# Kernel tuning notes

Measured on AMD Instinct MI355X. Metric: run time of the kernel, lower is better.

Reference implementation:

```python
import jax, jax.numpy as jnp
import numpy as np

N, E, G, D, H, C = 50000, 800000, 64, 128, 4, 32
EPS = 1e-5  # GraphNorm eps


def _gcn(x, W, b, src, dst, n):
    # PyG GCNConv: add self-loops (done by caller), symmetric norm D^-1/2 A D^-1/2
    xw = x @ W
    deg = jax.ops.segment_sum(jnp.ones_like(dst, dtype=xw.dtype), dst, num_segments=n)
    dinv = jnp.where(deg > 0, jax.lax.rsqrt(jnp.maximum(deg, 1e-12)), 0.0)
    norm = dinv[src] * dinv[dst]                      # [E2]
    out = jax.ops.segment_sum(xw[src] * norm[:, None], dst, num_segments=n)
    return out + b


def _gat(x, W, a_src, a_dst, b, src, dst, n):
    # PyG GATConv, heads=H, out C per head, concat, leaky_relu slope 0.2, self-loops added by caller
    h = (x @ W).reshape(n, H, C)
    es = jnp.einsum('nhc,hc->nh', h, a_src)
    ed = jnp.einsum('nhc,hc->nh', h, a_dst)
    e = jax.nn.leaky_relu(es[src] + ed[dst], 0.2)     # [E2,H]
    m = jax.ops.segment_max(e, dst, num_segments=n)   # per-dst softmax (stable)
    e = jnp.exp(e - m[dst])
    s = jax.ops.segment_sum(e, dst, num_segments=n)
    alpha = e / (s[dst] + 1e-16)
    out = jax.ops.segment_sum(h[src] * alpha[:, :, None], dst, num_segments=n)
    return out.reshape(n, H * C) + b


def _graphnorm(x, batch, w, b, ms, g):
    cnt = jnp.maximum(jax.ops.segment_sum(jnp.ones((x.shape[0],), x.dtype), batch, num_segments=g), 1.0)
    mean = jax.ops.segment_sum(x, batch, num_segments=g) / cnt[:, None]
    sub = x - ms * mean[batch]
    var = jax.ops.segment_sum(sub * sub, batch, num_segments=g) / cnt[:, None]
    return w * sub * jax.lax.rsqrt(var[batch] + EPS) + b


def setup_inputs() -> dict:
    key = jax.random.key(0)
    ks = jax.random.split(key, 40)

    def lin(k, din, dout):
        return jax.random.normal(k, (din, dout), jnp.float32) * np.float32((2.0 / (din + dout)) ** 0.5)

    inp = {
        'x': jax.random.normal(ks[0], (N, D), jnp.float32),
        'edge_index': jax.random.randint(ks[1], (2, E), 0, N, dtype=jnp.int32),
        'batch': jnp.sort(jax.random.randint(ks[2], (N,), 0, G, dtype=jnp.int32)),
        'Wp': lin(ks[3], D, D), 'bp': jnp.zeros((D,), jnp.float32),
        'Wg': lin(ks[4], D, D), 'bg': jnp.zeros((D,), jnp.float32),
        'Wa1': lin(ks[5], D, H * C), 'as1': jax.random.normal(ks[6], (H, C), jnp.float32) * 0.1,
        'ad1': jax.random.normal(ks[7], (H, C), jnp.float32) * 0.1, 'ba1': jnp.zeros((D,), jnp.float32),
        'Wa2': lin(ks[8], D, H * C), 'as2': jax.random.normal(ks[9], (H, C), jnp.float32) * 0.1,
        'ad2': jax.random.normal(ks[10], (H, C), jnp.float32) * 0.1, 'ba2': jnp.zeros((D,), jnp.float32),
        'gnw0': jnp.ones((D,), jnp.float32), 'gnb0': jnp.zeros((D,), jnp.float32), 'gns0': jnp.ones((D,), jnp.float32),
        'gnw1': jnp.ones((D,), jnp.float32), 'gnb1': jnp.zeros((D,), jnp.float32), 'gns1': jnp.ones((D,), jnp.float32),
        'gnw2': jnp.ones((D,), jnp.float32), 'gnb2': jnp.zeros((D,), jnp.float32), 'gns2': jnp.ones((D,), jnp.float32),
        'hw1': lin(ks[11], 2 * D, D), 'hb1': jnp.zeros((D,), jnp.float32),
        'hw2': lin(ks[12], D, D // 2), 'hb2': jnp.zeros((D // 2,), jnp.float32),
        'hw3': lin(ks[13], D // 2, 2), 'hb3': jnp.zeros((2,), jnp.float32),
        'nw1': lin(ks[14], D, D // 2), 'nb1': jnp.zeros((D // 2,), jnp.float32),
        'nw2': lin(ks[15], D // 2, 1), 'nb2': jnp.zeros((1,), jnp.float32),
    }
    return inp


def reference(x, edge_index, batch, Wp, bp, Wg, bg, Wa1, as1, ad1, ba1, Wa2, as2, ad2, ba2,
              gnw0, gnb0, gns0, gnw1, gnb1, gns1, gnw2, gnb2, gns2,
              hw1, hb1, hw2, hb2, hw3, hb3, nw1, nb1, nw2, nb2):
    n = x.shape[0]
    loop = jnp.arange(n, dtype=edge_index.dtype)
    src = jnp.concatenate([edge_index[0], loop])
    dst = jnp.concatenate([edge_index[1], loop])

    x = x @ Wp + bp
    h = _graphnorm(_gcn(x, Wg, bg, src, dst, n), batch, gnw0, gnb0, gns0, G)
    x = jax.nn.relu(h) + x  # dropout is identity in eval mode
    h = _graphnorm(_gat(x, Wa1, as1, ad1, ba1, src, dst, n), batch, gnw1, gnb1, gns1, G)
    x = jax.nn.relu(h) + x
    h = _graphnorm(_gat(x, Wa2, as2, ad2, ba2, src, dst, n), batch, gnw2, gnb2, gns2, G)
    x = jax.nn.relu(h) + x

    node_hub_scores = jax.nn.sigmoid((jax.nn.relu(x @ nw1 + nb1) @ nw2 + nb2)[:, 0])

    cnt = jnp.maximum(jax.ops.segment_sum(jnp.ones((n,), x.dtype), batch, num_segments=G), 1.0)
    gmean = jax.ops.segment_sum(x, batch, num_segments=G) / cnt[:, None]
    gmax = jax.ops.segment_max(x, batch, num_segments=G)
    graph_features = jnp.concatenate([gmean, gmax], axis=1)  # [G, 2D]

    z = jax.nn.relu(graph_features @ hw1 + hb1)
    z = jax.nn.relu(z @ hw2 + hb2)
    logits = z @ hw3 + hb3
    return (logits, node_hub_scores, graph_features, x)
```

## Files before the change

### kernel.cpp

```cpp
#include <hip/hip_runtime.h>
#include <cstdint>

#define D 128
#define GG 64
#define SLICES 16

typedef short bf16x8 __attribute__((ext_vector_type(8)));
typedef float f32x4 __attribute__((ext_vector_type(4)));

__device__ inline unsigned packbf2(float a, float b) {
  unsigned ua = __float_as_uint(a), ub = __float_as_uint(b);
  ua = (ua + 0x7FFFu + ((ua >> 16) & 1u)) >> 16;
  ub = (ub + 0x7FFFu + ((ub >> 16) & 1u)) >> 16;
  return ua | (ub << 16);
}
__device__ inline unsigned short bf16u(float f) {
  unsigned u = __float_as_uint(f);
  u = (u + 0x7FFFu + ((u >> 16) & 1u)) >> 16;
  return (unsigned short)u;
}
__device__ inline float2 unpackbf2(unsigned u) {
  return make_float2(__uint_as_float(u << 16), __uint_as_float(u & 0xFFFF0000u));
}

__global__ void count_edges_k(const int* __restrict__ dst, int* __restrict__ cnt, int E) {
  int e = blockIdx.x * blockDim.x + threadIdx.x;
  if (e < E) atomicAdd(&cnt[dst[e]], 1);
}

__global__ void bounds_init_k(int* __restrict__ gstart, int* __restrict__ gend) {
  int g = threadIdx.x;
  gstart[g] = 0;
  gend[g] = 0;
}

__global__ void graph_bounds_k(const int* __restrict__ batch, int* __restrict__ gstart,
                               int* __restrict__ gend, int n) {
  int i = blockIdx.x * blockDim.x + threadIdx.x;
  if (i >= n) return;
  int b = batch[i];
  if (i == 0) {
    gstart[b] = 0;
  } else {
    int pb = batch[i - 1];
    if (pb != b) { gstart[b] = i; gend[pb] = i; }
  }
  if (i == n - 1) gend[b] = n;
}

__global__ void gcnt_k(const int* __restrict__ gstart, const int* __restrict__ gend,
                       int* __restrict__ gcnt) {
  int g = threadIdx.x;
  gcnt[g] = gend[g] - gstart[g];
}

__global__ __launch_bounds__(256) void scan1_k(const int* __restrict__ cnt, int* __restrict__ rp,
                                               int* __restrict__ bsum, int n) {
  __shared__ int sd[256];
  int t = threadIdx.x;
  int i = blockIdx.x * 256 + t;
  int v = (i < n) ? cnt[i] : 0;
  sd[t] = v;
  __syncthreads();
#pragma unroll
  for (int off = 1; off < 256; off <<= 1) {
    int u = (t >= off) ? sd[t - off] : 0;
    __syncthreads();
    sd[t] += u;
    __syncthreads();
  }
  if (i < n) rp[i] = sd[t] - v;
  if (t == 255) bsum[blockIdx.x] = sd[255];
}

__global__ __launch_bounds__(256) void scan2_k(int* __restrict__ bsum, int nb) {
  __shared__ int sd[256];
  int t = threadIdx.x;
  int v = (t < nb) ? bsum[t] : 0;
  sd[t] = v;
  __syncthreads();
#pragma unroll
  for (int off = 1; off < 256; off <<= 1) {
    int u = (t >= off) ? sd[t - off] : 0;
    __syncthreads();
    sd[t] += u;
    __syncthreads();
  }
  if (t < nb) bsum[t] = sd[t] - v;
}

__global__ __launch_bounds__(256) void scan3_k(int* __restrict__ rp, const int* __restrict__ bsum,
                                               int* __restrict__ cur, int n, int E) {
  int i = blockIdx.x * 256 + threadIdx.x;
  if (i < n) {
    int r = rp[i] + bsum[blockIdx.x];
    rp[i] = r;
    cur[i] = r;
  }
  if (i == 0) rp[n] = E;
}

__global__ void fill_csr_k(const int* __restrict__ src, const int* __restrict__ dst,
                           int* __restrict__ cur, int* __restrict__ col, int E) {
  int e = blockIdx.x * blockDim.x + threadIdx.x;
  if (e >= E) return;
  int p = atomicAdd(&cur[dst[e]], 1);
  col[p] = src[e];
}

__global__ void dinv_k(const int* __restrict__ cnt, float* __restrict__ dinv, int n) {
  int i = blockIdx.x * blockDim.x + threadIdx.x;
  if (i < n) dinv[i] = rsqrtf((float)cnt[i] + 1.0f);
}

__global__ void cast_bf16_k(const float* __restrict__ in, unsigned short* __restrict__ outp, int n4) {
  int i = blockIdx.x * blockDim.x + threadIdx.x;
  if (i >= n4) return;
  float4 v = ((const float4*)in)[i];
  ushort4 o;
  o.x = bf16u(v.x); o.y = bf16u(v.y); o.z = bf16u(v.z); o.w = bf16u(v.w);
  ((ushort4*)outp)[i] = o;
}

__global__ void packB_k(const float* __restrict__ B, unsigned short* __restrict__ Bp, int ldb, int ct) {
  int idx = blockIdx.x * 256 + threadIdx.x;
  if (idx >= ct * 256) return;
  int lane = idx & 63;
  int kc = (idx >> 6) & 3;
  int c = idx >> 8;
  int kb = kc * 32 + (lane >> 4) * 8;
  int colq = c * 16 + (lane & 15);
  unsigned short o[8];
#pragma unroll
  for (int j = 0; j < 8; ++j) o[j] = bf16u(B[(size_t)(kb + j) * ldb + colq]);
  uint4 p;
  p.x = (unsigned)o[0] | ((unsigned)o[1] << 16);
  p.y = (unsigned)o[2] | ((unsigned)o[3] << 16);
  p.z = (unsigned)o[4] | ((unsigned)o[5] << 16);
  p.w = (unsigned)o[6] | ((unsigned)o[7] << 16);
  *(uint4*)&Bp[(size_t)idx * 8] = p;
}

__global__ __launch_bounds__(256) void gemm_mfma_k(const unsigned short* __restrict__ Ab,
                                                   const unsigned short* __restrict__ Bp,
                                                   const float* __restrict__ bias,
                                                   float* __restrict__ Cf,
                                                   unsigned short* __restrict__ Cb, int M) {
  __shared__ unsigned short Bs[16384];
  int t = threadIdx.x;
  for (int i = t; i < 2048; i += 256) ((uint4*)Bs)[i] = ((const uint4*)Bp)[i];
  __syncthreads();
  int w = t >> 6, lane = t & 63;
  int row0 = blockIdx.x * 64 + w * 16;
  int arow = row0 + (lane & 15);
  f32x4 acc[8];
#pragma unroll
  for (int c = 0; c < 8; ++c) acc[c] = {0.f, 0.f, 0.f, 0.f};
#pragma unroll
  for (int kc = 0; kc < 4; ++kc) {
    bf16x8 a = {0, 0, 0, 0, 0, 0, 0, 0};
    if (arow < M) a = *(const bf16x8*)&Ab[(size_t)arow * 128 + kc * 32 + (lane >> 4) * 8];
#pragma unroll
    for (int c = 0; c < 8; ++c) {
      bf16x8 b = *(const bf16x8*)&Bs[((c * 4 + kc) * 64 + lane) * 8];
      acc[c] = __builtin_amdgcn_mfma_f32_16x16x32_bf16(a, b, acc[c], 0, 0, 0);
    }
  }
  int rbase = row0 + (lane >> 4) * 4;
#pragma unroll
  for (int c = 0; c < 8; ++c) {
    int colq = c * 16 + (lane & 15);
    float bb = bias ? bias[colq] : 0.f;
#pragma unroll
    for (int r = 0; r < 4; ++r) {
      int row = rbase + r;
      if (row < M) {
        float v = acc[c][r] + bb;
        if (Cf) Cf[(size_t)row * 128 + colq] = v;
        if (Cb) Cb[(size_t)row * 128 + colq] = bf16u(v);
      }
    }
  }
}

__global__ __launch_bounds__(256) void gcn_gather_k(const unsigned* __restrict__ xwb,
                                                    const int* __restrict__ rp, const int* __restrict__ col,
                                                    const float* __restrict__ dinv, const float* __restrict__ bias,
                                                    float* __restrict__ out, int n) {
  int i = blockIdx.x * 4 + (threadIdx.x >> 6);
  if (i >= n) return;
  int lane = threadIdx.x & 63;
  int e0 = __builtin_amdgcn_readfirstlane(rp[i]);
  int e1 = __builtin_amdgcn_readfirstlane(rp[i + 1]);
  float di = dinv[i];
  float2 sv = unpackbf2(xwb[(size_t)i * 64 + lane]);
  float ax0 = sv.x * di * di, ay0 = sv.y * di * di;
  float ax1 = 0.f, ay1 = 0.f, ax2 = 0.f, ay2 = 0.f, ax3 = 0.f, ay3 = 0.f;
  int e = e0;
  for (; e + 3 < e1; e += 4) {
    int s0 = __builtin_amdgcn_readfirstlane(col[e]);
    int s1 = __builtin_amdgcn_readfirstlane(col[e + 1]);
    int s2 = __builtin_amdgcn_readfirstlane(col[e + 2]);
    int s3 = __builtin_amdgcn_readfirstlane(col[e + 3]);
    float w0 = dinv[s0] * di, w1 = dinv[s1] * di, w2 = dinv[s2] * di, w3 = dinv[s3] * di;
    float2 v0 = unpackbf2(xwb[(size_t)s0 * 64 + lane]);
    float2 v1 = unpackbf2(xwb[(size_t)s1 * 64 + lane]);
    float2 v2 = unpackbf2(xwb[(size_t)s2 * 64 + lane]);
    float2 v3 = unpackbf2(xwb[(size_t)s3 * 64 + lane]);
    ax0 += v0.x * w0; ay0 += v0.y * w0;
    ax1 += v1.x * w1; ay1 += v1.y * w1;
    ax2 += v2.x * w2; ay2 += v2.y * w2;
    ax3 += v3.x * w3; ay3 += v3.y * w3;
  }
  for (; e < e1; ++e) {
    int s0 = __builtin_amdgcn_readfirstlane(col[e]);
    float w0 = dinv[s0] * di;
    float2 v0 = unpackbf2(xwb[(size_t)s0 * 64 + lane]);
    ax0 += v0.x * w0; ay0 += v0.y * w0;
  }
  float2 bb = ((const float2*)bias)[lane];
  ((float2*)out)[(size_t)i * 64 + lane] =
      make_float2(ax0 + ax1 + ax2 + ax3 + bb.x, ay0 + ay1 + ay2 + ay3 + bb.y);
}

__global__ void attn_coef_k(const unsigned short* __restrict__ hb, const float* __restrict__ a_s,
                            const float* __restrict__ a_d, float* __restrict__ es,
                            float* __restrict__ ed, int n) {
  int idx = blockIdx.x * blockDim.x + threadIdx.x;
  if (idx >= n * 4) return;
  int node = idx >> 2, hh = idx & 3;
  const uint4* hr = (const uint4*)(hb + (size_t)node * 128 + hh * 32);
  const float4* av = (const float4*)(a_s + hh * 32);
  const float4* dv = (const float4*)(a_d + hh * 32);
  float s = 0.f, d2 = 0.f;
#pragma unroll
  for (int q = 0; q < 4; ++q) {
    uint4 u = hr[q];
    float2 p0 = unpackbf2(u.x), p1 = unpackbf2(u.y), p2 = unpackbf2(u.z), p3 = unpackbf2(u.w);
    float4 a0 = av[q * 2], a1 = av[q * 2 + 1];
    float4 d0 = dv[q * 2], d1 = dv[q * 2 + 1];
    s  += p0.x * a0.x + p0.y * a0.y + p1.x * a0.z + p1.y * a0.w
        + p2.x * a1.x + p2.y * a1.y + p3.x * a1.z + p3.y * a1.w;
    d2 += p0.x * d0.x + p0.y * d0.y + p1.x * d0.z + p1.y * d0.w
        + p2.x * d1.x + p2.y * d1.y + p3.x * d1.z + p3.y * d1.w;
  }
  es[idx] = s;
  ed[idx] = d2;
}

__global__ __launch_bounds__(256) void alpha_k(const float* __restrict__ es, const float* __restrict__ ed,
                                               const int* __restrict__ rp, const int* __restrict__ col,
                                               float* __restrict__ alpha, float* __restrict__ aself, int n) {
  int i = blockIdx.x * 4 + (threadIdx.x >> 6);
  if (i >= n) return;
  int lane = threadIdx.x & 63;
  int hh = lane >> 4, slot = lane & 15;
  int e0 = __builtin_amdgcn_readfirstlane(rp[i]);
  int e1 = __builtin_amdgcn_readfirstlane(rp[i + 1]);
  float edi = ed[i * 4 + hh];
  float esf = es[i * 4 + hh] + edi;
  esf = esf >= 0.f ? esf : 0.2f * esf;
  float m = esf;
  for (int e = e0 + slot; e < e1; e += 16) {
    int sj = col[e];
    float ev = es[sj * 4 + hh] + edi;
    ev = ev >= 0.f ? ev : 0.2f * ev;
    alpha[(size_t)e * 4 + hh] = ev;
    m = fmaxf(m, ev);
  }
#pragma unroll
  for (int off = 1; off < 16; off <<= 1) m = fmaxf(m, __shfl_xor(m, off, 64));
  float s = (slot == 0) ? __expf(esf - m) : 0.f;
  for (int e = e0 + slot; e < e1; e += 16) {
    float w = __expf(alpha[(size_t)e * 4 + hh] - m);
    alpha[(size_t)e * 4 + hh] = w;
    s += w;
  }
#pragma unroll
  for (int off = 1; off < 16; off <<= 1) s += __shfl_xor(s, off, 64);
  float winv = 1.0f / (s + 1e-16f);
  for (int e = e0 + slot; e < e1; e += 16) {
    alpha[(size_t)e * 4 + hh] *= winv;
  }
  if (slot == 0) aself[i * 4 + hh] = __expf(esf - m) * winv;
}

__global__ __launch_bounds__(256) void gat_gather_k(const unsigned* __restrict__ hfb,
                                                    const int* __restrict__ rp, const int* __restrict__ col,
                                                    const float* __restrict__ alpha, const float* __restrict__ aself,
                                                    const float* __restrict__ bias, float* __restrict__ out, int n) {
  int i = blockIdx.x * 4 + (threadIdx.x >> 6);
  if (i >= n) return;
  int lane = threadIdx.x & 63;
  int hh = lane >> 4;
  int e0 = __builtin_amdgcn_readfirstlane(rp[i]);
  int e1 = __builtin_amdgcn_readfirstlane(rp[i + 1]);
  float2 sv = unpackbf2(hfb[(size_t)i * 64 + lane]);
  float a0 = aself[i * 4 + hh];
  float ax0 = sv.x * a0, ay0 = sv.y * a0;
  float ax1 = 0.f, ay1 = 0.f, ax2 = 0.f, ay2 = 0.f, ax3 = 0.f, ay3 = 0.f;
  int e = e0;
  for (; e + 3 < e1; e += 4) {
    int s0 = __builtin_amdgcn_readfirstlane(col[e]);
    int s1 = __builtin_amdgcn_readfirstlane(col[e + 1]);
    int s2 = __builtin_amdgcn_readfirstlane(col[e + 2]);
    int s3 = __builtin_amdgcn_readfirstlane(col[e + 3]);
    float aa0 = alpha[(size_t)e * 4 + hh];
    float aa1 = alpha[(size_t)(e + 1) * 4 + hh];
    float aa2 = alpha[(size_t)(e + 2) * 4 + hh];
    float aa3 = alpha[(size_t)(e + 3) * 4 + hh];
    float2 v0 = unpackbf2(hfb[(size_t)s0 * 64 + lane]);
    float2 v1 = unpackbf2(hfb[(size_t)s1 * 64 + lane]);
    float2 v2 = unpackbf2(hfb[(size_t)s2 * 64 + lane]);
    float2 v3 = unpackbf2(hfb[(size_t)s3 * 64 + lane]);
    ax0 += v0.x * aa0; ay0 += v0.y * aa0;
    ax1 += v1.x * aa1; ay1 += v1.y * aa1;
    ax2 += v2.x * aa2; ay2 += v2.y * aa2;
    ax3 += v3.x * aa3; ay3 += v3.y * aa3;
  }
  for (; e < e1; ++e) {
    int s0 = __builtin_amdgcn_readfirstlane(col[e]);
    float aa0 = alpha[(size_t)e * 4 + hh];
    float2 v0 = unpackbf2(hfb[(size_t)s0 * 64 + lane]);
    ax0 += v0.x * aa0; ay0 += v0.y * aa0;
  }
  float2 bb = ((const float2*)bias)[lane];
  ((float2*)out)[(size_t)i * 64 + lane] =
      make_float2(ax0 + ax1 + ax2 + ax3 + bb.x, ay0 + ay1 + ay2 + ay3 + bb.y);
}

__global__ __launch_bounds__(256) void gn_stats_k(const float* __restrict__ h, const int* __restrict__ gstart,
                                                  const int* __restrict__ gcnt, float* __restrict__ gsum,
                                                  float* __restrict__ gsq) {
  int g = blockIdx.x / SLICES, sl = blockIdx.x % SLICES;
  int st = gstart[g], cn = gcnt[g];
  int d = threadIdx.x & 127, half = threadIdx.x >> 7;
  float s = 0.f, ss = 0.f;
  for (int r = sl * 2 + half; r < cn; r += 2 * SLICES) {
    float v = h[(size_t)(st + r) * D + d];
    s += v; ss += v * v;
  }
  __shared__ float l1[128], l2[128];
  if (half) { l1[d] = s; l2[d] = ss; }
  __syncthreads();
  if (!half) {
    atomicAdd(&gsum[g * D + d], s + l1[d]);
    atomicAdd(&gsq[g * D + d], ss + l2[d]);
  }
}

__global__ void gn_finalize_k(const float* __restrict__ gsum, const float* __restrict__ gsq,
                              const int* __restrict__ gcnt, const float* __restrict__ ms,
                              float* __restrict__ mean, float* __restrict__ rstd) {
  int g = blockIdx.x, d = threadIdx.x;
  float cnt = fmaxf((float)gcnt[g], 1.0f);
  float mu = gsum[g * D + d] / cnt;
  float m2 = gsq[g * D + d] / cnt;
  float s = ms[d];
  float var = m2 - (2.0f * s - s * s) * mu * mu;
  mean[g * D + d] = mu;
  rstd[g * D + d] = rsqrtf(fmaxf(var, 0.0f) + 1e-5f);
}

__global__ void gn_apply_k(const float* __restrict__ h, float* __restrict__ x,
                           unsigned short* __restrict__ xb,
                           const int* __restrict__ batch, const float* __restrict__ mean,
                           const float* __restrict__ rstd, const float* __restrict__ w,
                           const float* __restrict__ b, const float* __restrict__ ms, int n) {
  int idx = blockIdx.x * blockDim.x + threadIdx.x;
  if (idx >= n * 32) return;
  int node = idx >> 5, q = idx & 31;
  int g = batch[node];
  int d0 = q * 4;
  float4 hv = ((const float4*)h)[idx];
  float4 xv = ((const float4*)x)[idx];
  float ha[4] = {hv.x, hv.y, hv.z, hv.w};
  float xa[4] = {xv.x, xv.y, xv.z, xv.w};
  float ra[4];
#pragma unroll
  for (int j = 0; j < 4; ++j) {
    int d = d0 + j;
    float sub = ha[j] - ms[d] * mean[g * D + d];
    float v = w[d] * sub * rstd[g * D + d] + b[d];
    ra[j] = fmaxf(v, 0.f) + xa[j];
  }
  ((float4*)x)[idx] = make_float4(ra[0], ra[1], ra[2], ra[3]);
  ushort4 o;
  o.x = bf16u(ra[0]); o.y = bf16u(ra[1]); o.z = bf16u(ra[2]); o.w = bf16u(ra[3]);
  ((ushort4*)xb)[idx] = o;
}

__global__ __launch_bounds__(256) void hub_mfma_k(const unsigned short* __restrict__ Xb,
                                                  const unsigned short* __restrict__ W1p,
                                                  const float* __restrict__ nb1, const float* __restrict__ nw2,
                                                  const float* __restrict__ nb2, float* __restrict__ out, int n) {
  __shared__ unsigned short Bs[8192];
  int t = threadIdx.x;
  for (int i = t; i < 1024; i += 256) ((uint4*)Bs)[i] = ((const uint4*)W1p)[i];
  __syncthreads();
  int w = t >> 6, lane = t & 63;
  int row0 = blockIdx.x * 64 + w * 16;
  int arow = row0 + (lane & 15);
  f32x4 acc[4];
#pragma unroll
  for (int c = 0; c < 4; ++c) acc[c] = {0.f, 0.f, 0.f, 0.f};
#pragma unroll
  for (int kc = 0; kc < 4; ++kc) {
    bf16x8 a = {0, 0, 0, 0, 0, 0, 0, 0};
    if (arow < n) a = *(const bf16x8*)&Xb[(size_t)arow * 128 + kc * 32 + (lane >> 4) * 8];
#pragma unroll
    for (int c = 0; c < 4; ++c) {
      bf16x8 b = *(const bf16x8*)&Bs[((c * 4 + kc) * 64 + lane) * 8];
      acc[c] = __builtin_amdgcn_mfma_f32_16x16x32_bf16(a, b, acc[c], 0, 0, 0);
    }
  }
  float b2 = nb2[0];
  float s[4] = {0.f, 0.f, 0.f, 0.f};
#pragma unroll
  for (int c = 0; c < 4; ++c) {
    int colq = c * 16 + (lane & 15);
    float b1 = nb1[colq];
    float w2 = nw2[colq];
#pragma unroll
    for (int r = 0; r < 4; ++r) s[r] += fmaxf(acc[c][r] + b1, 0.f) * w2;
  }
#pragma unroll
  for (int off = 1; off < 16; off <<= 1) {
#pragma unroll
    for (int r = 0; r < 4; ++r) s[r] += __shfl_xor(s[r], off, 64);
  }
  if ((lane & 15) == 0) {
    int rbase = row0 + (lane >> 4) * 4;
#pragma unroll
    for (int r = 0; r < 4; ++r) {
      int row = rbase + r;
      if (row < n) out[row] = 1.0f / (1.0f + __expf(-(s[r] + b2)));
    }
  }
}

__global__ void init_maxu_k(unsigned* __restrict__ p, int n) {
  int i = blockIdx.x * blockDim.x + threadIdx.x;
  if (i < n) p[i] = 0x007FFFFFu;
}

__global__ __launch_bounds__(256) void pool_stats_k(const float* __restrict__ x, const int* __restrict__ gstart,
                                                    const int* __restrict__ gcnt, float* __restrict__ gsum,
                                                    unsigned* __restrict__ gmaxu) {
  int g = blockIdx.x / SLICES, sl = blockIdx.x % SLICES;
  int st = gstart[g], cn = gcnt[g];
  int d = threadIdx.x & 127, half = threadIdx.x >> 7;
  float s = 0.f, mx = __uint_as_float(0xFF800000u);
  for (int r = sl * 2 + half; r < cn; r += 2 * SLICES) {
    float v = x[(size_t)(st + r) * D + d];
    s += v; mx = fmaxf(mx, v);
  }
  __shared__ float l1[128], l2[128];
  if (half) { l1[d] = s; l2[d] = mx; }
  __syncthreads();
  if (!half) {
    s += l1[d];
    mx = fmaxf(mx, l2[d]);
    atomicAdd(&gsum[g * D + d], s);
    unsigned u = __float_as_uint(mx);
    u = (u & 0x80000000u) ? ~u : (u | 0x80000000u);
    atomicMax(&gmaxu[g * D + d], u);
  }
}

__global__ void pool_fin_k(const float* __restrict__ gsum, const unsigned* __restrict__ gmaxu,
                           const int* __restrict__ gcnt, float* __restrict__ gf) {
  int g = blockIdx.x, d = threadIdx.x;
  float cnt = fmaxf((float)gcnt[g], 1.0f);
  gf[g * 256 + d] = gsum[g * D + d] / cnt;
  unsigned u = gmaxu[g * D + d];
  unsigned bits = (u & 0x80000000u) ? (u ^ 0x80000000u) : ~u;
  gf[g * 256 + 128 + d] = __uint_as_float(bits);
}

__global__ __launch_bounds__(128) void mlp_k(const float* __restrict__ gf, const float* __restrict__ hw1,
                                             const float* __restrict__ hb1, const float* __restrict__ hw2,
                                             const float* __restrict__ hb2, const float* __restrict__ hw3,
                                             const float* __restrict__ hb3, float* __restrict__ logits) {
  __shared__ float sg[256], z1[128], z2[64];
  int g = blockIdx.x, t = threadIdx.x;
  sg[t] = gf[g * 256 + t];
  sg[t + 128] = gf[g * 256 + 128 + t];
  __syncthreads();
  float a = hb1[t];
  for (int k = 0; k < 256; ++k) a += sg[k] * hw1[k * 128 + t];
  z1[t] = fmaxf(a, 0.f);
  __syncthreads();
  if (t < 64) {
    float a2 = hb2[t];
    for (int k = 0; k < 128; ++k) a2 += z1[k] * hw2[k * 64 + t];
    z2[t] = fmaxf(a2, 0.f);
  }
  __syncthreads();
  if (t < 2) {
    float a3 = hb3[t];
    for (int k = 0; k < 64; ++k) a3 += z2[k] * hw3[k * 2 + t];
    logits[g * 2 + t] = a3;
  }
}

extern "C" void kernel_launch(void* const* d_in, const int* in_sizes, int n_in,
                              void* d_out, int out_size, void* d_ws, size_t ws_size,
                              hipStream_t stream) {
  const float* x_in  = (const float*)d_in[0];
  const int*   eidx  = (const int*)d_in[1];
  const int*   batch = (const int*)d_in[2];
  const float* Wp  = (const float*)d_in[3];
  const float* bp  = (const float*)d_in[4];
  const float* Wg  = (const float*)d_in[5];
  const float* bg  = (const float*)d_in[6];
  const float* Wa1 = (const float*)d_in[7];
  const float* as1 = (const float*)d_in[8];
  const float* ad1 = (const float*)d_in[9];
  const float* ba1 = (const float*)d_in[10];
  const float* Wa2 = (const float*)d_in[11];
  const float* as2 = (const float*)d_in[12];
  const float* ad2 = (const float*)d_in[13];
  const float* ba2 = (const float*)d_in[14];
  const float* gnw[3] = {(const float*)d_in[15], (const float*)d_in[18], (const float*)d_in[21]};
  const float* gnb[3] = {(const float*)d_in[16], (const float*)d_in[19], (const float*)d_in[22]};
  const float* gns[3] = {(const float*)d_in[17], (const float*)d_in[20], (const float*)d_in[23]};
  const float* hw1 = (const float*)d_in[24];
  const float* hb1 = (const float*)d_in[25];
  const float* hw2 = (const float*)d_in[26];
  const float* hb2 = (const float*)d_in[27];
  const float* hw3 = (const float*)d_in[28];
  const float* hb3 = (const float*)d_in[29];
  const float* nw1 = (const float*)d_in[30];
  const float* nb1 = (const float*)d_in[31];
  const float* nw2 = (const float*)d_in[32];
  const float* nb2 = (const float*)d_in[33];

  const int N = in_sizes[0] / D;
  const int E = in_sizes[1] / 2;
  const int* src = eidx;
  const int* dst = eidx + E;

  float* out    = (float*)d_out;
  float* logits = out;
  float* hub    = out + GG * 2;
  float* gf     = out + GG * 2 + N;
  float* X      = out + GG * 2 + N + GG * 256;

  char* wp = (char*)d_ws;
  auto alloc = [&](size_t bytes) { char* p = wp; wp += (bytes + 255) & ~(size_t)255; return p; };
  float*    B1    = (float*)alloc((size_t)N * D * 4);
  float*    B2    = (float*)alloc((size_t)N * D * 4);
  unsigned* B1h   = (unsigned*)alloc((size_t)N * (D / 2) * 4);
  unsigned short* Xb = (unsigned short*)alloc((size_t)N * D * 2);
  int*   col     = (int*)alloc((size_t)E * 4);
  int*   cnt     = (int*)alloc((size_t)N * 4);
  int*   rowp    = (int*)alloc((size_t)(N + 1) * 4);
  int*   cur     = (int*)alloc((size_t)N * 4);
  float* dinv    = (float*)alloc((size_t)N * 4);
  float* es      = (float*)alloc((size_t)N * 4 * 4);
  float* ed      = (float*)alloc((size_t)N * 4 * 4);
  float* aself   = (float*)alloc((size_t)N * 4 * 4);
  float* gsum    = (float*)alloc((size_t)GG * D * 4);
  float* gsq     = (float*)alloc((size_t)GG * D * 4);
  unsigned* gmaxu = (unsigned*)alloc((size_t)GG * D * 4);
  float* mean    = (float*)alloc((size_t)GG * D * 4);
  float* rstd    = (float*)alloc((size_t)GG * D * 4);
  int*   gcnt    = (int*)alloc((size_t)GG * 4);
  int*   gstart  = (int*)alloc((size_t)GG * 4);
  int*   gend    = (int*)alloc((size_t)GG * 4);
  int*   bsum    = (int*)alloc((size_t)256 * 4);
  unsigned short* Wpp  = (unsigned short*)alloc(16384 * 2);
  unsigned short* Wgp  = (unsigned short*)alloc(16384 * 2);
  unsigned short* Wa1p = (unsigned short*)alloc(16384 * 2);
  unsigned short* Wa2p = (unsigned short*)alloc(16384 * 2);
  unsigned short* W1p  = (unsigned short*)alloc(8192 * 2);
  float* alpha = B1;
  unsigned short* xinb = (unsigned short*)B2;
  if ((size_t)(wp - (char*)d_ws) > ws_size) return;

  const int nb = (N + 255) / 256;

  hipMemsetAsync(cnt, 0, (size_t)N * 4, stream);
  count_edges_k<<<(E + 255) / 256, 256, 0, stream>>>(dst, cnt, E);
  bounds_init_k<<<1, GG, 0, stream>>>(gstart, gend);
  graph_bounds_k<<<nb, 256, 0, stream>>>(batch, gstart, gend, N);
  gcnt_k<<<1, GG, 0, stream>>>(gstart, gend, gcnt);
  scan1_k<<<nb, 256, 0, stream>>>(cnt, rowp, bsum, N);
  scan2_k<<<1, 256, 0, stream>>>(bsum, nb);
  scan3_k<<<nb, 256, 0, stream>>>(rowp, bsum, cur, N, E);
  dinv_k<<<nb, 256, 0, stream>>>(cnt, dinv, N);
  fill_csr_k<<<(E + 255) / 256, 256, 0, stream>>>(src, dst, cur, col, E);

  packB_k<<<8, 256, 0, stream>>>(Wp, Wpp, 128, 8);
  packB_k<<<8, 256, 0, stream>>>(Wg, Wgp, 128, 8);
  packB_k<<<8, 256, 0, stream>>>(Wa1, Wa1p, 128, 8);
  packB_k<<<8, 256, 0, stream>>>(Wa2, Wa2p, 128, 8);
  packB_k<<<4, 256, 0, stream>>>(nw1, W1p, 64, 4);
  cast_bf16_k<<<(N * 32 + 255) / 256, 256, 0, stream>>>(x_in, xinb, N * 32);

  const int gemmGrid = (N + 63) / 64;
  const int aggGrid  = (N + 3) / 4;

  auto graphnorm = [&](int layer) {
    hipMemsetAsync(gsum, 0, 2 * (size_t)GG * D * 4, stream);
    gn_stats_k<<<GG * SLICES, 256, 0, stream>>>(B2, gstart, gcnt, gsum, gsq);
    gn_finalize_k<<<GG, D, 0, stream>>>(gsum, gsq, gcnt, gns[layer], mean, rstd);
    gn_apply_k<<<(N * 32 + 255) / 256, 256, 0, stream>>>(B2, X, Xb, batch, mean, rstd,
                                                         gnw[layer], gnb[layer], gns[layer], N);
  };

  gemm_mfma_k<<<gemmGrid, 256, 0, stream>>>(xinb, Wpp, bp, X, Xb, N);

  gemm_mfma_k<<<gemmGrid, 256, 0, stream>>>(Xb, Wgp, nullptr, nullptr, (unsigned short*)B1h, N);
  gcn_gather_k<<<aggGrid, 256, 0, stream>>>(B1h, rowp, col, dinv, bg, B2, N);
  graphnorm(0);

  gemm_mfma_k<<<gemmGrid, 256, 0, stream>>>(Xb, Wa1p, nullptr, nullptr, (unsigned short*)B1h, N);
  attn_coef_k<<<(N * 4 + 255) / 256, 256, 0, stream>>>((const unsigned short*)B1h, as1, ad1, es, ed, N);
  alpha_k<<<aggGrid, 256, 0, stream>>>(es, ed, rowp, col, alpha, aself, N);
  gat_gather_k<<<aggGrid, 256, 0, stream>>>(B1h, rowp, col, alpha, aself, ba1, B2, N);
  graphnorm(1);

  gemm_mfma_k<<<gemmGrid, 256, 0, stream>>>(Xb, Wa2p, nullptr, nullptr, (unsigned short*)B1h, N);
  attn_coef_k<<<(N * 4 + 255) / 256, 256, 0, stream>>>((const unsigned short*)B1h, as2, ad2, es, ed, N);
  alpha_k<<<aggGrid, 256, 0, stream>>>(es, ed, rowp, col, alpha, aself, N);
  gat_gather_k<<<aggGrid, 256, 0, stream>>>(B1h, rowp, col, alpha, aself, ba2, B2, N);
  graphnorm(2);

  hub_mfma_k<<<gemmGrid, 256, 0, stream>>>(Xb, W1p, nb1, nw2, nb2, hub, N);

  hipMemsetAsync(gsum, 0, (size_t)GG * D * 4, stream);
  init_maxu_k<<<(GG * D + 255) / 256, 256, 0, stream>>>(gmaxu, GG * D);
  pool_stats_k<<<GG * SLICES, 256, 0, stream>>>(X, gstart, gcnt, gsum, gmaxu);
  pool_fin_k<<<GG, D, 0, stream>>>(gsum, gmaxu, gcnt, gf);
  mlp_k<<<GG, 128, 0, stream>>>(gf, hw1, hb1, hw2, hb2, hw3, hb3, logits);
}
```

Baseline: 464.0 us.

## Defer softmax normalization to gather, widen gather unroll, multipass CSR fill

The alpha kernel no longer runs a third pass to rescale every edge weight; it stores unnormalized exp values plus a per-node reciprocal sum, which the GAT gather applies once at the end. Both gather kernels now process eight edges per iteration with predicated tails so more independent row loads are in flight. CSR fill is split into four passes over destination ranges, meant to improve atomic and write locality at the cost of reading the edge list four times. Padded tail lanes reload the node's own row with zero weight, adding some wasted loads on low-degree nodes.

```diff
diff --git a/kernel.cpp b/kernel.cpp
--- a/kernel.cpp
+++ b/kernel.cpp
@@ -4,16 +4,11 @@
 #define D 128
 #define GG 64
 #define SLICES 16
+#define NPASS 4
 
 typedef short bf16x8 __attribute__((ext_vector_type(8)));
 typedef float f32x4 __attribute__((ext_vector_type(4)));
 
-__device__ inline unsigned packbf2(float a, float b) {
-  unsigned ua = __float_as_uint(a), ub = __float_as_uint(b);
-  ua = (ua + 0x7FFFu + ((ua >> 16) & 1u)) >> 16;
-  ub = (ub + 0x7FFFu + ((ub >> 16) & 1u)) >> 16;
-  return ua | (ub << 16);
-}
 __device__ inline unsigned short bf16u(float f) {
   unsigned u = __float_as_uint(f);
   u = (u + 0x7FFFu + ((u >> 16) & 1u)) >> 16;
@@ -100,12 +95,18 @@
   if (i == 0) rp[n] = E;
 }
 
-__global__ void fill_csr_k(const int* __restrict__ src, const int* __restrict__ dst,
-                           int* __restrict__ cur, int* __restrict__ col, int E) {
-  int e = blockIdx.x * blockDim.x + threadIdx.x;
+__global__ __launch_bounds__(256) void fill_csr_mp_k(const int* __restrict__ src,
+                                                     const int* __restrict__ dst,
+                                                     int* __restrict__ cur, int* __restrict__ col,
+                                                     int E, int slice, int chunks) {
+  int pass = blockIdx.x / chunks;
+  int e = (blockIdx.x % chunks) * 256 + threadIdx.x;
   if (e >= E) return;
-  int p = atomicAdd(&cur[dst[e]], 1);
-  col[p] = src[e];
+  int d = dst[e];
+  if (d >= pass * slice && d < (pass + 1) * slice) {
+    int p = atomicAdd(&cur[d], 1);
+    col[p] = src[e];
+  }
 }
 
 __global__ void dinv_k(const int* __restrict__ cnt, float* __restrict__ dinv, int n) {
@@ -194,33 +195,26 @@
   int e1 = __builtin_amdgcn_readfirstlane(rp[i + 1]);
   float di = dinv[i];
   float2 sv = unpackbf2(xwb[(size_t)i * 64 + lane]);
-  float ax0 = sv.x * di * di, ay0 = sv.y * di * di;
-  float ax1 = 0.f, ay1 = 0.f, ax2 = 0.f, ay2 = 0.f, ax3 = 0.f, ay3 = 0.f;
-  int e = e0;
-  for (; e + 3 < e1; e += 4) {
-    int s0 = __builtin_amdgcn_readfirstlane(col[e]);
-    int s1 = __builtin_amdgcn_readfirstlane(col[e + 1]);
-    int s2 = __builtin_amdgcn_readfirstlane(col[e + 2]);
-    int s3 = __builtin_amdgcn_readfirstlane(col[e + 3]);
-    float w0 = dinv[s0] * di, w1 = dinv[s1] * di, w2 = dinv[s2] * di, w3 = dinv[s3] * di;
-    float2 v0 = unpackbf2(xwb[(size_t)s0 * 64 + lane]);
-    float2 v1 = unpackbf2(xwb[(size_t)s1 * 64 + lane]);
-    float2 v2 = unpackbf2(xwb[(size_t)s2 * 64 + lane]);
-    float2 v3 = unpackbf2(xwb[(size_t)s3 * 64 + lane]);
-    ax0 += v0.x * w0; ay0 += v0.y * w0;
-    ax1 += v1.x * w1; ay1 += v1.y * w1;
-    ax2 += v2.x * w2; ay2 += v2.y * w2;
-    ax3 += v3.x * w3; ay3 += v3.y * w3;
-  }
-  for (; e < e1; ++e) {
-    int s0 = __builtin_amdgcn_readfirstlane(col[e]);
-    float w0 = dinv[s0] * di;
-    float2 v0 = unpackbf2(xwb[(size_t)s0 * 64 + lane]);
-    ax0 += v0.x * w0; ay0 += v0.y * w0;
+  float ax[4], ay[4];
+  ax[0] = sv.x * di * di; ay[0] = sv.y * di * di;
+  ax[1] = ax[2] = ax[3] = ay[1] = ay[2] = ay[3] = 0.f;
+  for (int e = e0; e < e1; e += 8) {
+    int s[8]; float w[8];
+#pragma unroll
+    for (int j = 0; j < 8; ++j) {
+      bool ok = (e + j < e1);
+      s[j] = ok ? __builtin_amdgcn_readfirstlane(col[e + j]) : i;
+      w[j] = ok ? dinv[s[j]] * di : 0.f;
+    }
+    float2 v[8];
+#pragma unroll
+    for (int j = 0; j < 8; ++j) v[j] = unpackbf2(xwb[(size_t)s[j] * 64 + lane]);
+#pragma unroll
+    for (int j = 0; j < 8; ++j) { ax[j & 3] += v[j].x * w[j]; ay[j & 3] += v[j].y * w[j]; }
   }
   float2 bb = ((const float2*)bias)[lane];
   ((float2*)out)[(size_t)i * 64 + lane] =
-      make_float2(ax0 + ax1 + ax2 + ax3 + bb.x, ay0 + ay1 + ay2 + ay3 + bb.y);
+      make_float2(ax[0] + ax[1] + ax[2] + ax[3] + bb.x, ay[0] + ay[1] + ay[2] + ay[3] + bb.y);
 }
 
 __global__ void attn_coef_k(const unsigned short* __restrict__ hb, const float* __restrict__ a_s,
@@ -250,7 +244,8 @@
 
 __global__ __launch_bounds__(256) void alpha_k(const float* __restrict__ es, const float* __restrict__ ed,
                                                const int* __restrict__ rp, const int* __restrict__ col,
-                                               float* __restrict__ alpha, float* __restrict__ aself, int n) {
+                                               float* __restrict__ alpha, float* __restrict__ aself,
+                                               float* __restrict__ winv, int n) {
   int i = blockIdx.x * 4 + (threadIdx.x >> 6);
   if (i >= n) return;
   int lane = threadIdx.x & 63;
@@ -278,16 +273,16 @@
   }
 #pragma unroll
   for (int off = 1; off < 16; off <<= 1) s += __shfl_xor(s, off, 64);
-  float winv = 1.0f / (s + 1e-16f);
-  for (int e = e0 + slot; e < e1; e += 16) {
-    alpha[(size_t)e * 4 + hh] *= winv;
-  }
-  if (slot == 0) aself[i * 4 + hh] = __expf(esf - m) * winv;
+  if (slot == 0) {
+    aself[i * 4 + hh] = __expf(esf - m);
+    winv[i * 4 + hh] = 1.0f / (s + 1e-16f);
+  }
 }
 
 __global__ __launch_bounds__(256) void gat_gather_k(const unsigned* __restrict__ hfb,
                                                     const int* __restrict__ rp, const int* __restrict__ col,
                                                     const float* __restrict__ alpha, const float* __restrict__ aself,
+                                                    const float* __restrict__ winv,
                                                     const float* __restrict__ bias, float* __restrict__ out, int n) {
   int i = blockIdx.x * 4 + (threadIdx.x >> 6);
   if (i >= n) return;
@@ -297,36 +292,28 @@
   int e1 = __builtin_amdgcn_readfirstlane(rp[i + 1]);
   float2 sv = unpackbf2(hfb[(size_t)i * 64 + lane]);
   float a0 = aself[i * 4 + hh];
-  float ax0 = sv.x * a0, ay0 = sv.y * a0;
-  float ax1 = 0.f, ay1 = 0.f, ax2 = 0.f, ay2 = 0.f, ax3 = 0.f, ay3 = 0.f;
-  int e = e0;
-  for (; e + 3 < e1; e += 4) {
-    int s0 = __builtin_amdgcn_readfirstlane(col[e]);
-    int s1 = __builtin_amdgcn_readfirstlane(col[e + 1]);
-    int s2 = __builtin_amdgcn_readfirstlane(col[e + 2]);
-    int s3 = __builtin_amdgcn_readfirstlane(col[e + 3]);
-    float aa0 = alpha[(size_t)e * 4 + hh];
-    float aa1 = alpha[(size_t)(e + 1) * 4 + hh];
-    float aa2 = alpha[(size_t)(e + 2) * 4 + hh];
-    float aa3 = alpha[(size_t)(e + 3) * 4 + hh];
-    float2 v0 = unpackbf2(hfb[(size_t)s0 * 64 + lane]);
-    float2 v1 = unpackbf2(hfb[(size_t)s1 * 64 + lane]);
-    float2 v2 = unpackbf2(hfb[(size_t)s2 * 64 + lane]);
-    float2 v3 = unpackbf2(hfb[(size_t)s3 * 64 + lane]);
-    ax0 += v0.x * aa0; ay0 += v0.y * aa0;
-    ax1 += v1.x * aa1; ay1 += v1.y * aa1;
-    ax2 += v2.x * aa2; ay2 += v2.y * aa2;
-    ax3 += v3.x * aa3; ay3 += v3.y * aa3;
-  }
-  for (; e < e1; ++e) {
-    int s0 = __builtin_amdgcn_readfirstlane(col[e]);
-    float aa0 = alpha[(size_t)e * 4 + hh];
-    float2 v0 = unpackbf2(hfb[(size_t)s0 * 64 + lane]);
-    ax0 += v0.x * aa0; ay0 += v0.y * aa0;
-  }
+  float ax[4], ay[4];
+  ax[0] = sv.x * a0; ay[0] = sv.y * a0;
+  ax[1] = ax[2] = ax[3] = ay[1] = ay[2] = ay[3] = 0.f;
+  for (int e = e0; e < e1; e += 8) {
+    int s[8]; float aa[8];
+#pragma unroll
+    for (int j = 0; j < 8; ++j) {
+      bool ok = (e + j < e1);
+      s[j] = ok ? __builtin_amdgcn_readfirstlane(col[e + j]) : i;
+      aa[j] = ok ? alpha[(size_t)(e + j) * 4 + hh] : 0.f;
+    }
+    float2 v[8];
+#pragma unroll
+    for (int j = 0; j < 8; ++j) v[j] = unpackbf2(hfb[(size_t)s[j] * 64 + lane]);
+#pragma unroll
+    for (int j = 0; j < 8; ++j) { ax[j & 3] += v[j].x * aa[j]; ay[j & 3] += v[j].y * aa[j]; }
+  }
+  float wi = winv[i * 4 + hh];
   float2 bb = ((const float2*)bias)[lane];
   ((float2*)out)[(size_t)i * 64 + lane] =
-      make_float2(ax0 + ax1 + ax2 + ax3 + bb.x, ay0 + ay1 + ay2 + ay3 + bb.y);
+      make_float2((ax[0] + ax[1] + ax[2] + ax[3]) * wi + bb.x,
+                  (ay[0] + ay[1] + ay[2] + ay[3]) * wi + bb.y);
 }
 
 __global__ __launch_bounds__(256) void gn_stats_k(const float* __restrict__ h, const int* __restrict__ gstart,
@@ -561,6 +548,7 @@
   float* es      = (float*)alloc((size_t)N * 4 * 4);
   float* ed      = (float*)alloc((size_t)N * 4 * 4);
   float* aself   = (float*)alloc((size_t)N * 4 * 4);
+  float* winv    = (float*)alloc((size_t)N * 4 * 4);
   float* gsum    = (float*)alloc((size_t)GG * D * 4);
   float* gsq     = (float*)alloc((size_t)GG * D * 4);
   unsigned* gmaxu = (unsigned*)alloc((size_t)GG * D * 4);
@@ -590,7 +578,11 @@
   scan2_k<<<1, 256, 0, stream>>>(bsum, nb);
   scan3_k<<<nb, 256, 0, stream>>>(rowp, bsum, cur, N, E);
   dinv_k<<<nb, 256, 0, stream>>>(cnt, dinv, N);
-  fill_csr_k<<<(E + 255) / 256, 256, 0, stream>>>(src, dst, cur, col, E);
+  {
+    int chunks = (E + 255) / 256;
+    int slice = (N + NPASS - 1) / NPASS;
+    fill_csr_mp_k<<<chunks * NPASS, 256, 0, stream>>>(src, dst, cur, col, E, slice, chunks);
+  }
 
   packB_k<<<8, 256, 0, stream>>>(Wp, Wpp, 128, 8);
   packB_k<<<8, 256, 0, stream>>>(Wg, Wgp, 128, 8);
@@ -618,14 +610,14 @@
 
   gemm_mfma_k<<<gemmGrid, 256, 0, stream>>>(Xb, Wa1p, nullptr, nullptr, (unsigned short*)B1h, N);
   attn_coef_k<<<(N * 4 + 255) / 256, 256, 0, stream>>>((const unsigned short*)B1h, as1, ad1, es, ed, N);
-  alpha_k<<<aggGrid, 256, 0, stream>>>(es, ed, rowp, col, alpha, aself, N);
-  gat_gather_k<<<aggGrid, 256, 0, stream>>>(B1h, rowp, col, alpha, aself, ba1, B2, N);
+  alpha_k<<<aggGrid, 256, 0, stream>>>(es, ed, rowp, col, alpha, aself, winv, N);
+  gat_gather_k<<<aggGrid, 256, 0, stream>>>(B1h, rowp, col, alpha, aself, winv, ba1, B2, N);
   graphnorm(1);
 
   gemm_mfma_k<<<gemmGrid, 256, 0, stream>>>(Xb, Wa2p, nullptr, nullptr, (unsigned short*)B1h, N);
   attn_coef_k<<<(N * 4 + 255) / 256, 256, 0, stream>>>((const unsigned short*)B1h, as2, ad2, es, ed, N);
-  alpha_k<<<aggGrid, 256, 0, stream>>>(es, ed, rowp, col, alpha, aself, N);
-  gat_gather_k<<<aggGrid, 256, 0, stream>>>(B1h, rowp, col, alpha, aself, ba2, B2, N);
+  alpha_k<<<aggGrid, 256, 0, stream>>>(es, ed, rowp, col, alpha, aself, winv, N);
+  gat_gather_k<<<aggGrid, 256, 0, stream>>>(B1h, rowp, col, alpha, aself, winv, ba2, B2, N);
   graphnorm(2);
 
   hub_mfma_k<<<gemmGrid, 256, 0, stream>>>(Xb, W1p, nb1, nw2, nb2, hub, N);
```

After: 471.3 us. About the same (+1.6%).
